# Performance work log

Hardware: AMD Instinct MI355X
Metric: run time of the kernel (lower is better)

## Reference

```python
import jax, jax.numpy as jnp
import numpy as np

IMG_H, IMG_W = 240, 320
NEAR, FAR = 0.1, 10.0
CHUNK = 64  # triangles rasterized per scan step
CAM_K = np.array([[286.2057, 0.0, 162.6306],
                  [0.0, 286.7852, 121.0245],
                  [0.0, 0.0, 1.0]], np.float32)


def build_projection(cam, w, h, x0=0, y0=0, nc=NEAR, fc=FAR):
    q = -(fc + nc) / float(fc - nc)
    qn = -2.0 * fc * nc / float(fc - nc)
    proj = np.array([
        [2 * cam[0, 0] / w, -2 * cam[0, 1] / w, (-2 * cam[0, 2] + w + 2 * x0) / w, 0],
        [0, -2 * cam[1, 1] / h, (-2 * cam[1, 2] + h + 2 * y0) / h, 0],
        [0, 0, q, qn],
        [0, 0, -1, 0]], dtype=np.float64)
    proj[1, :] *= -1.0
    return jnp.asarray(proj.T, jnp.float32)


def vertex_normals(verts, faces):
    # per-face normal scattered to its vertices then renormalized
    # (equals dirt lighting.vertex_normals_pre_split on split meshes)
    v0, v1, v2 = verts[faces[:, 0]], verts[faces[:, 1]], verts[faces[:, 2]]
    fn = jnp.cross(v1 - v0, v2 - v0)
    fn = fn / jnp.maximum(jnp.linalg.norm(fn, axis=1, keepdims=True), 1e-12)
    vn = (jnp.zeros_like(verts)
          .at[faces[:, 0]].add(fn)
          .at[faces[:, 1]].add(fn)
          .at[faces[:, 2]].add(fn))
    return vn / jnp.maximum(jnp.linalg.norm(vn, axis=1, keepdims=True), 1e-12)


def transform_vertices(vertices, pose, faces, proj):
    vert_obj = jnp.concatenate([vertices, jnp.ones_like(vertices[:, -1:])], axis=1)  # [V,4]
    normals = vertex_normals(vert_obj[:, :3], faces)
    gl = jnp.array([[1., 0., 0.], [0., -1., 0.], [0., 0., -1.]], jnp.float32)
    rot = gl @ pose[:3, :3]
    # replicate the flat-list surgery: cam_pose[:3,:3]=gl@R, negate t_y, t_z
    cam_pose = pose.at[:3, :3].set(rot).at[1, 3].multiply(-1.0).at[2, 3].multiply(-1.0)
    view = cam_pose.T
    vert_cam = vert_obj @ view                                   # [V,4]
    vert_3d = vert_obj[:, :3] @ pose[:3, :3].T + pose[:3, 3]     # [V,3]
    vert_clip = vert_cam @ proj                                  # [V,4]
    return vert_obj, vert_3d, vert_clip, normals


def rasterise(vert_clip, colors, faces, H, W):
    # z-buffered triangle rasterization with perspective-correct barycentric
    # interpolation, processed in chunks of CHUNK triangles via lax.scan.
    eps = 1e-9
    wc = vert_clip[:, 3]
    inv_w = 1.0 / jnp.where(jnp.abs(wc) > eps, wc, eps)
    ndc = vert_clip[:, :3] * inv_w[:, None]
    px = (ndc[:, 0] + 1.0) * 0.5 * W   # screen x
    py = (1.0 - ndc[:, 1]) * 0.5 * H   # screen y (row 0 at top)
    pz = ndc[:, 2]

    tpx, tpy, tpz = px[faces], py[faces], pz[faces]   # [F,3]
    tiw = inv_w[faces]                                # [F,3]
    tcol = colors[faces]                              # [F,3,C]
    tval = jnp.all(wc[faces] > 1e-6, axis=1)          # all verts in front

    F = faces.shape[0]
    pad = (-F) % CHUNK
    def padf(a):
        if pad == 0:
            return a
        return jnp.concatenate([a, jnp.zeros((pad,) + a.shape[1:], a.dtype)], 0)
    tpx, tpy, tpz, tiw, tcol = padf(tpx), padf(tpy), padf(tpz), padf(tiw), padf(tcol)
    tval = padf(tval)
    n_steps = (F + pad) // CHUNK
    resh = lambda a: a.reshape((n_steps, CHUNK) + a.shape[1:])
    xs = tuple(map(resh, (tpx, tpy, tpz, tiw, tcol, tval)))

    Xg = (jnp.arange(W, dtype=jnp.float32) + 0.5)[None, :, None]  # pixel centers
    Yg = (jnp.arange(H, dtype=jnp.float32) + 0.5)[:, None, None]
    BIG = jnp.float32(1e9)

    def step(carry, chunk):
        zbuf, cbuf = carry
        cpx, cpy, cpz, ciw, ccol, cval = chunk
        ax, ay = cpx[:, 0], cpy[:, 0]
        bx, by = cpx[:, 1], cpy[:, 1]
        cx, cy = cpx[:, 2], cpy[:, 2]
        area = (bx - ax) * (cy - ay) - (by - ay) * (cx - ax)            # [Fc]
        inv_area = 1.0 / jnp.where(jnp.abs(area) > 1e-12, area, 1e-12)
        # normalized edge functions (barycentrics), [H,W,Fc]
        e0 = ((Xg - bx) * (cy - by) - (Yg - by) * (cx - bx)) * inv_area
        e1 = ((Xg - cx) * (ay - cy) - (Yg - cy) * (ax - cx)) * inv_area
        e2 = 1.0 - e0 - e1
        depth = e0 * cpz[:, 0] + e1 * cpz[:, 1] + e2 * cpz[:, 2]        # screen-linear z
        inside = ((e0 >= 0) & (e1 >= 0) & (e2 >= 0) & cval
                  & (jnp.abs(area) > 1e-12) & (depth >= -1.0) & (depth <= 1.0))
        dmask = jnp.where(inside, depth, BIG)
        best = jnp.argmin(dmask, axis=2)                                # [H,W]
        bidx = best[..., None]
        bdepth = jnp.take_along_axis(dmask, bidx, 2)[..., 0]
        take = bdepth < zbuf
        b0 = jnp.take_along_axis(e0, bidx, 2)[..., 0]
        b1 = jnp.take_along_axis(e1, bidx, 2)[..., 0]
        b2 = 1.0 - b0 - b1
        piw = jnp.stack([b0, b1, b2], -1) * ciw[best]                   # [H,W,3]
        den = jnp.sum(piw, -1, keepdims=True)
        den = jnp.where(jnp.abs(den) > 1e-12, den, 1e-12)
        col = jnp.einsum('hwk,hwkc->hwc', piw / den, ccol[best])        # persp-correct
        zbuf = jnp.where(take, bdepth, zbuf)
        cbuf = jnp.where(take[..., None], col, cbuf)
        return (zbuf, cbuf), None

    zbuf0 = jnp.full((H, W), BIG, jnp.float32)
    cbuf0 = jnp.zeros((H, W, colors.shape[1]), jnp.float32)
    (_, cbuf), _ = jax.lax.scan(jax.checkpoint(step), (zbuf0, cbuf0), xs)
    return cbuf


def setup_inputs() -> dict:
    key = jax.random.key(0)
    k1, k2 = jax.random.split(key)
    V, F = 12288, 4096
    vertices = 0.15 * jax.random.normal(k1, (1, V, 3), jnp.float32)
    faces = jax.random.randint(k2, (1, F, 3), 0, V, jnp.int32)
    pose = jnp.eye(4, dtype=jnp.float32).at[2, 3].set(0.6)  # object 0.6m in front
    return {"vertices": vertices, "faces": faces, "poses": pose[None]}


def reference(vertices, faces, poses):
    proj = build_projection(CAM_K, IMG_W, IMG_H)
    faces0 = jnp.asarray(faces[0], jnp.int32)
    vert_obj, vert_3d, vert_clip, normals = transform_vertices(vertices[0], poses[0], faces0, proj)
    colors = jnp.concatenate(
        [jnp.ones_like(vert_obj[:, :1]), vert_3d, normals, vert_obj], axis=1)  # [V,11]
    g = rasterise(vert_clip, colors, faces0, IMG_H, IMG_W)  # [H,W,11]
    return g[None]
```

## Files before the change

kernel.cpp:

```cpp
#include <hip/hip_runtime.h>
#include <math.h>

#pragma clang fp contract(off)

#define IMG_H 240
#define IMG_W 320
#define NPX   (IMG_H * IMG_W)
#define NCH   11
#define NCHP  12
#define NSLICE 8
#define CULL_M 1e-3f
#define EZ_M   1e-5f

struct ProjM { float m[16]; };

extern "C" __global__ void k_init(float* __restrict__ vnacc, int n3v,
                                  unsigned long long* __restrict__ zkey) {
  int i = blockIdx.x * 256 + threadIdx.x;
  if (i < n3v) vnacc[i] = 0.0f;
  if (i < NPX) zkey[i] = ~0ull;
}

__device__ __forceinline__ void xform(float x, float y, float z,
                                      const float* __restrict__ pose,
                                      const ProjM& P,
                                      float& px, float& py, float& pz,
                                      float& iw, float& wc) {
  float c0 = ((x*pose[0]     + y*pose[1])     + z*pose[2])     + pose[3];
  float c1 = ((x*(-pose[4])  + y*(-pose[5]))  + z*(-pose[6]))  + (-pose[7]);
  float c2 = ((x*(-pose[8])  + y*(-pose[9]))  + z*(-pose[10])) + (-pose[11]);
  float c3 = ((x*pose[12]    + y*pose[13])    + z*pose[14])    + pose[15];
  float q0 = ((c0*P.m[0]  + c1*P.m[1])  + c2*P.m[2])  + c3*P.m[3];
  float q1 = ((c0*P.m[4]  + c1*P.m[5])  + c2*P.m[6])  + c3*P.m[7];
  float q2 = ((c0*P.m[8]  + c1*P.m[9])  + c2*P.m[10]) + c3*P.m[11];
  float q3 = ((c0*P.m[12] + c1*P.m[13]) + c2*P.m[14]) + c3*P.m[15];
  wc = q3;
  float denw = (fabsf(wc) > 1e-9f) ? wc : 1e-9f;
  iw = 1.0f / denw;
  float ndx = q0 * iw, ndy = q1 * iw;
  pz = q2 * iw;
  px = ((ndx + 1.0f) * 0.5f) * (float)IMG_W;
  py = ((1.0f - ndy) * 0.5f) * (float)IMG_H;
}

extern "C" __global__ void k_face(const float* __restrict__ verts,
                                  const int* __restrict__ faces,
                                  const float* __restrict__ pose,
                                  ProjM P,
                                  float* __restrict__ vnacc,
                                  float4* __restrict__ frec,
                                  float4* __restrict__ fbb,
                                  float4* __restrict__ fe,
                                  int4*  __restrict__ fidx, int F) {
  int f = blockIdx.x * 64 + threadIdx.x;
  if (f >= F) return;
  int i0 = faces[3*f+0], i1 = faces[3*f+1], i2 = faces[3*f+2];
  float x0 = verts[3*i0+0], y0 = verts[3*i0+1], z0 = verts[3*i0+2];
  float x1 = verts[3*i1+0], y1 = verts[3*i1+1], z1 = verts[3*i1+2];
  float x2 = verts[3*i2+0], y2 = verts[3*i2+1], z2 = verts[3*i2+2];

  {
    float ux = x1 - x0, uy = y1 - y0, uz = z1 - z0;
    float vx = x2 - x0, vy = y2 - y0, vz = z2 - z0;
    float fx = uy*vz - uz*vy;
    float fy = uz*vx - ux*vz;
    float fz = ux*vy - uy*vx;
    float n = sqrtf((fx*fx + fy*fy) + fz*fz);
    float d = fmaxf(n, 1e-12f);
    fx = fx / d; fy = fy / d; fz = fz / d;
    atomicAdd(&vnacc[3*i0+0], fx); atomicAdd(&vnacc[3*i0+1], fy); atomicAdd(&vnacc[3*i0+2], fz);
    atomicAdd(&vnacc[3*i1+0], fx); atomicAdd(&vnacc[3*i1+1], fy); atomicAdd(&vnacc[3*i1+2], fz);
    atomicAdd(&vnacc[3*i2+0], fx); atomicAdd(&vnacc[3*i2+1], fy); atomicAdd(&vnacc[3*i2+2], fz);
  }

  float ax, ay, pz0, iw0, w0;  xform(x0, y0, z0, pose, P, ax, ay, pz0, iw0, w0);
  float bx, by, pz1, iw1, w1;  xform(x1, y1, z1, pose, P, bx, by, pz1, iw1, w1);
  float cx, cy, pz2, iw2, w2;  xform(x2, y2, z2, pose, P, cx, cy, pz2, iw2, w2);

  float area = (bx - ax) * (cy - ay) - (by - ay) * (cx - ax);
  float inva = 1.0f / ((fabsf(area) > 1e-12f) ? area : 1e-12f);
  bool valid = (w0 > 1e-6f) && (w1 > 1e-6f) && (w2 > 1e-6f) && (fabsf(area) > 1e-12f);
  float rax = 2.0f*cx - ax, ray = 2.0f*cy - ay;
  float rbx = 2.0f*cx - bx, rby = 2.0f*cy - by;
  float minx = fminf(cx, fminf(rax, rbx)), maxx = fmaxf(cx, fmaxf(rax, rbx));
  float miny = fminf(cy, fminf(ray, rby)), maxy = fmaxf(cy, fmaxf(ray, rby));
  frec[4*f+0] = make_float4(bx, by, cy - by, cx - bx);
  frec[4*f+1] = make_float4(cx, cy, ay - cy, ax - cx);
  frec[4*f+2] = make_float4(inva, pz0, pz1, pz2);
  frec[4*f+3] = make_float4(iw0, iw1, iw2, 0.0f);
  fbb[f] = valid ? make_float4(minx, maxx, miny, maxy)
                 : make_float4(1e30f, -1e30f, 1e30f, -1e30f);
  fidx[f] = make_int4(i0, i1, i2, 0);
  {
    double dbx = bx, dby = by, dcx = cx, dcy = cy, dax = ax, day = ay;
    double dinv = (double)inva;
    double d0 = dcy - dby, d1 = dcx - dbx;
    double d2 = day - dcy, d3 = dax - dcx;
    double a0 = d0 * dinv, b0 = -d1 * dinv, c0 = (dby * d1 - dbx * d0) * dinv;
    double a1 = d2 * dinv, b1 = -d3 * dinv, c1 = (dcy * d3 - dcx * d2) * dinv;
    fe[2*f+0] = make_float4((float)a0, (float)b0, (float)c0, 0.0f);
    fe[2*f+1] = make_float4((float)a1, (float)b1, (float)c1, 0.0f);
  }
}

extern "C" __global__ void k_vertex(const float* __restrict__ verts,
                                    const float* __restrict__ vnacc,
                                    const float* __restrict__ pose,
                                    float4* __restrict__ colors, int V) {
  int i = blockIdx.x * 64 + threadIdx.x;
  if (i >= V) return;
  float x = verts[3*i+0], y = verts[3*i+1], z = verts[3*i+2];

  float nx = vnacc[3*i+0], ny = vnacc[3*i+1], nz = vnacc[3*i+2];
  float nn = sqrtf((nx*nx + ny*ny) + nz*nz);
  float nm = fmaxf(nn, 1e-12f);
  nx = nx / nm; ny = ny / nm; nz = nz / nm;

  float v3x = ((x*pose[0] + y*pose[1]) + z*pose[2])  + pose[3];
  float v3y = ((x*pose[4] + y*pose[5]) + z*pose[6])  + pose[7];
  float v3z = ((x*pose[8] + y*pose[9]) + z*pose[10]) + pose[11];

  colors[3*i+0] = make_float4(1.0f, v3x, v3y, v3z);
  colors[3*i+1] = make_float4(nx, ny, nz, x);
  colors[3*i+2] = make_float4(y, z, 1.0f, 0.0f);
}

extern "C" __global__ __launch_bounds__(256)
void k_rasterA(const float4* __restrict__ frec,
               const float4* __restrict__ fbb,
               const float4* __restrict__ fe,
               unsigned long long* __restrict__ zkey,
               int F, int nslice) {
  int t = threadIdx.x;
  int wave = t >> 6;
  int lane = t & 63;
  int sx = (wave & 1) * 8, sy = (wave >> 1) * 8;
  int pxi = blockIdx.x * 16 + sx + (lane & 7);
  int pyi = blockIdx.y * 16 + sy + (lane >> 3);
  float X = (float)pxi + 0.5f;
  float Y = (float)pyi + 0.5f;
  float tXlo = (float)(blockIdx.x * 16 + sx) + 0.5f, tXhi = tXlo + 7.0f;
  float tYlo = (float)(blockIdx.y * 16 + sy) + 0.5f, tYhi = tYlo + 7.0f;

  int f0 = blockIdx.z * nslice;
  int f1 = min(F, f0 + nslice);

  float bestd = 1e9f;
  int   besti = -1;

  for (int base = f0; base < f1; base += 64) {
    int f = base + lane;
    bool ov = false;
    if (f < f1) {
      float4 bb = fbb[f];
      ov = (bb.x - 1.0f <= tXhi) && (bb.y + 1.0f >= tXlo) &&
           (bb.z - 1.0f <= tYhi) && (bb.w + 1.0f >= tYlo);
      if (ov) {
        float4 E0 = fe[2*f+0];
        float4 E1 = fe[2*f+1];
        float pa0 = E0.x * tXlo, pb0 = E0.x * tXhi;
        float qa0 = E0.y * tYlo, qb0 = E0.y * tYhi;
        float e0mx = (fmaxf(pa0, pb0) + fmaxf(qa0, qb0)) + E0.z;
        float e0mn = (fminf(pa0, pb0) + fminf(qa0, qb0)) + E0.z;
        float pa1 = E1.x * tXlo, pb1 = E1.x * tXhi;
        float qa1 = E1.y * tYlo, qb1 = E1.y * tYhi;
        float e1mx = (fmaxf(pa1, pb1) + fmaxf(qa1, qb1)) + E1.z;
        float e1mn = (fminf(pa1, pb1) + fminf(qa1, qb1)) + E1.z;
        float e2mx = (1.0f - e0mn) - e1mn;
        ov = (e0mx >= -CULL_M) && (e1mx >= -CULL_M) && (e2mx >= -CULL_M);
      }
    }
    unsigned long long mask = __ballot(ov);

    while (mask) {
      int j = __builtin_ctzll(mask);
      mask &= mask - 1;
      int ju = __builtin_amdgcn_readfirstlane(base + j);
      const float4* fr = frec + (size_t)ju * 4;
      float4 C = fr[2];
      float zminf = fminf(C.y, fminf(C.z, C.w));
      if (__ballot(bestd > zminf - EZ_M) == 0ull) continue;
      float4 A = fr[0];
      float4 B = fr[1];
      float t0 = (X - A.x) * A.z;
      float t1 = (Y - A.y) * A.w;
      float e0 = (t0 - t1) * C.x;
      float t2 = (X - B.x) * B.z;
      float t3 = (Y - B.y) * B.w;
      float e1 = (t2 - t3) * C.x;
      float e2 = (1.0f - e0) - e1;
      float depth = ((e0 * C.y) + (e1 * C.z)) + (e2 * C.w);
      bool inside = (e0 >= 0.0f) && (e1 >= 0.0f) && (e2 >= 0.0f) &&
                    (depth >= -1.0f) && (depth <= 1.0f);
      if (inside && depth < bestd) {
        bestd = depth; besti = base + j;
      }
    }
  }

  if (besti >= 0) {
    unsigned int ub = __float_as_uint(bestd);
    ub = (ub & 0x80000000u) ? ~ub : (ub | 0x80000000u);
    unsigned long long key = ((unsigned long long)ub << 32) | (unsigned int)besti;
    atomicMin(&zkey[(size_t)pyi * IMG_W + pxi], key);
  }
}

extern "C" __global__ __launch_bounds__(256)
void k_resolve(const unsigned long long* __restrict__ zkey,
               const float4* __restrict__ frec,
               const float4* __restrict__ colors,
               const int4* __restrict__ fidx,
               float* __restrict__ out) {
  __shared__ float sOut[256 * NCH];
  int t = threadIdx.x;
  int p = blockIdx.x * 256 + t;
  int pyi = p / IMG_W, pxi = p - pyi * IMG_W;
  float X = (float)pxi + 0.5f;
  float Y = (float)pyi + 0.5f;
  unsigned long long key = zkey[p];

  float oc[NCH];
  if (key != ~0ull) {
    int besti = (int)(key & 0xFFFFFFFFu);
    const float4* fr = frec + (size_t)besti * 4;
    float4 A = fr[0], B = fr[1], C = fr[2], D = fr[3];
    float t0 = (X - A.x) * A.z;
    float t1 = (Y - A.y) * A.w;
    float e0 = (t0 - t1) * C.x;
    float t2 = (X - B.x) * B.z;
    float t3 = (Y - B.y) * B.w;
    float e1 = (t2 - t3) * C.x;
    float b2 = (1.0f - e0) - e1;
    float p0 = e0 * D.x, p1 = e1 * D.y, p2 = b2 * D.z;
    float den = (p0 + p1) + p2;
    if (!(fabsf(den) > 1e-12f)) den = 1e-12f;
    float u0 = p0 / den, u1 = p1 / den, u2 = p2 / den;
    int4 vi = fidx[besti];
    float c0v[NCHP], c1v[NCHP], c2v[NCHP];
    #pragma unroll
    for (int k = 0; k < 3; ++k) {
      *(float4*)(c0v + 4*k) = colors[3*vi.x + k];
      *(float4*)(c1v + 4*k) = colors[3*vi.y + k];
      *(float4*)(c2v + 4*k) = colors[3*vi.z + k];
    }
    #pragma unroll
    for (int ch = 0; ch < NCH; ++ch)
      oc[ch] = (u0 * c0v[ch] + u1 * c1v[ch]) + u2 * c2v[ch];
  } else {
    #pragma unroll
    for (int ch = 0; ch < NCH; ++ch) oc[ch] = 0.0f;
  }
  #pragma unroll
  for (int ch = 0; ch < NCH; ++ch) sOut[t * NCH + ch] = oc[ch];
  __syncthreads();
  float4* o4 = (float4*)(out + (size_t)blockIdx.x * 256 * NCH);
  const float4* s4 = (const float4*)sOut;
  #pragma unroll
  for (int k = 0; k < 3; ++k) {
    int idx = t + k * 256;
    if (idx < 704) o4[idx] = s4[idx];
  }
}

extern "C" void kernel_launch(void* const* d_in, const int* in_sizes, int n_in,
                              void* d_out, int out_size, void* d_ws, size_t ws_size,
                              hipStream_t stream) {
  const float* verts = (const float*)d_in[0];
  const int*   faces = (const int*)d_in[1];
  const float* pose  = (const float*)d_in[2];
  float* out = (float*)d_out;
  int V = in_sizes[0] / 3;
  int F = in_sizes[1] / 3;

  float* ws = (float*)d_ws;
  size_t o = 0;
  auto alloc = [&](size_t n) { size_t r = o; o += (n + 3) & ~(size_t)3; return r; };
  size_t o_zk   = alloc((size_t)2 * NPX);
  size_t o_vn   = alloc((size_t)3 * V);
  size_t o_col  = alloc((size_t)NCHP * V);
  size_t o_fr   = alloc((size_t)16 * F);
  size_t o_bb   = alloc((size_t)4 * F);
  size_t o_fe   = alloc((size_t)8 * F);
  size_t o_fi   = alloc((size_t)4 * F);
  unsigned long long* zkey = (unsigned long long*)(ws + o_zk);
  float*  vnacc = ws + o_vn;
  float4* col   = (float4*)(ws + o_col);
  float4* frec  = (float4*)(ws + o_fr);
  float4* fbb   = (float4*)(ws + o_bb);
  float4* fe    = (float4*)(ws + o_fe);
  int4*   fidx  = (int4*)(ws + o_fi);

  double fxd = 286.2057, sd = 0.0, cxd = 162.6306;
  double fyd = 286.7852, cyd = 121.0245;
  double wd = IMG_W, hd = IMG_H, ncd = 0.1, fcd = 10.0;
  double q  = -(fcd + ncd) / (fcd - ncd);
  double qn = -2.0 * fcd * ncd / (fcd - ncd);
  double Pd[16] = {
    2.0*fxd/wd, -2.0*sd/wd, (-2.0*cxd + wd)/wd, 0.0,
    0.0,        2.0*fyd/hd, (2.0*cyd - hd)/hd, -0.0,
    0.0,        0.0,        q,                  qn,
    0.0,        0.0,       -1.0,                0.0 };
  ProjM P;
  for (int i = 0; i < 16; ++i) P.m[i] = (float)Pd[i];

  int n3v = 3 * V;
  int initN = (NPX > n3v) ? NPX : n3v;
  k_init<<<(initN + 255) / 256, 256, 0, stream>>>(vnacc, n3v, zkey);
  k_face<<<(F + 63) / 64, 64, 0, stream>>>(verts, faces, pose, P, vnacc,
                                           frec, fbb, fe, fidx, F);
  k_vertex<<<(V + 63) / 64, 64, 0, stream>>>(verts, vnacc, pose, col, V);
  int nslice = (F + NSLICE - 1) / NSLICE;
  dim3 g(IMG_W / 16, IMG_H / 16, NSLICE);
  k_rasterA<<<g, 256, 0, stream>>>(frec, fbb, fe, zkey, F, nslice);
  k_resolve<<<NPX / 256, 256, 0, stream>>>(zkey, frec, col, fidx, out);
}
```

Measured before the change: 90.49 us.

## Sort faces front-to-back by depth bins and early-exit raster loop

Faces are bucketed into 256 bins by their minimum NDC depth using a histogram, a prefix scan and a scatter, so the rasterizer walks them roughly front to back. Each raster wave interleaves chunks across z-slices, reads the current per-pixel best depth from the global z-key buffer, and breaks once the remaining chunks' bin lower bound exceeds the wave's worst best depth. It also skips individual faces whose min depth cannot win. This adds three small kernels, extra global memory traffic and per-chunk atomics in exchange for culling occluded triangles.

```diff
diff --git a/kernel.cpp b/kernel.cpp
--- a/kernel.cpp
+++ b/kernel.cpp
@@ -11,14 +11,24 @@
 #define NSLICE 8
 #define CULL_M 1e-3f
 #define EZ_M   1e-5f
+#define NBIN   256
 
 struct ProjM { float m[16]; };
 
+__device__ __forceinline__ int zbin(float zm) {
+  float t = fminf(fmaxf((zm + 1.0f) * 128.0f, 0.0f), 255.0f);
+  int b = (int)t;
+  if ((float)b * 0.0078125f - 1.0f > zm) b = (b > 0) ? b - 1 : 0;
+  return b;
+}
+
 extern "C" __global__ void k_init(float* __restrict__ vnacc, int n3v,
-                                  unsigned long long* __restrict__ zkey) {
+                                  unsigned long long* __restrict__ zkey,
+                                  int* __restrict__ hist) {
   int i = blockIdx.x * 256 + threadIdx.x;
   if (i < n3v) vnacc[i] = 0.0f;
   if (i < NPX) zkey[i] = ~0ull;
+  if (i < NBIN) hist[i] = 0;
 }
 
 __device__ __forceinline__ void xform(float x, float y, float z,
@@ -51,7 +61,9 @@
                                   float4* __restrict__ frec,
                                   float4* __restrict__ fbb,
                                   float4* __restrict__ fe,
-                                  int4*  __restrict__ fidx, int F) {
+                                  int4*  __restrict__ fidx,
+                                  float* __restrict__ fzmin,
+                                  int*   __restrict__ hist, int F) {
   int f = blockIdx.x * 64 + threadIdx.x;
   if (f >= F) return;
   int i0 = faces[3*f+0], i1 = faces[3*f+1], i2 = faces[3*f+2];
@@ -91,6 +103,11 @@
   fbb[f] = valid ? make_float4(minx, maxx, miny, maxy)
                  : make_float4(1e30f, -1e30f, 1e30f, -1e30f);
   fidx[f] = make_int4(i0, i1, i2, 0);
+
+  float zm = valid ? fminf(pz0, fminf(pz1, pz2)) : __builtin_huge_valf();
+  fzmin[f] = zm;
+  atomicAdd(&hist[zbin(zm)], 1);
+
   {
     double dbx = bx, dby = by, dcx = cx, dcy = cy, dax = ax, day = ay;
     double dinv = (double)inva;
@@ -103,6 +120,44 @@
   }
 }
 
+extern "C" __global__ void k_scan(const int* __restrict__ hist,
+                                  int* __restrict__ binoff) {
+  __shared__ int s[NBIN];
+  int t = threadIdx.x;
+  int v = hist[t];
+  s[t] = v;
+  __syncthreads();
+  for (int o = 1; o < NBIN; o <<= 1) {
+    int x = (t >= o) ? s[t - o] : 0;
+    __syncthreads();
+    s[t] += x;
+    __syncthreads();
+  }
+  binoff[t] = s[t] - v;
+}
+
+extern "C" __global__ void k_scatter(const float* __restrict__ fzmin,
+                                     int* __restrict__ binoff,
+                                     const float4* __restrict__ fbb,
+                                     const float4* __restrict__ fe,
+                                     int*   __restrict__ forig,
+                                     float* __restrict__ szmin,
+                                     float* __restrict__ smon,
+                                     float4* __restrict__ fbbs,
+                                     float4* __restrict__ fes, int F) {
+  int f = blockIdx.x * 256 + threadIdx.x;
+  if (f >= F) return;
+  float zm = fzmin[f];
+  int b = zbin(zm);
+  int pos = atomicAdd(&binoff[b], 1);
+  forig[pos] = f;
+  szmin[pos] = zm;
+  smon[pos]  = (float)b * 0.0078125f - 1.0f;
+  fbbs[pos]  = fbb[f];
+  fes[2*pos+0] = fe[2*f+0];
+  fes[2*pos+1] = fe[2*f+1];
+}
+
 extern "C" __global__ void k_vertex(const float* __restrict__ verts,
                                     const float* __restrict__ vnacc,
                                     const float* __restrict__ pose,
@@ -127,10 +182,13 @@
 
 extern "C" __global__ __launch_bounds__(256)
 void k_rasterA(const float4* __restrict__ frec,
-               const float4* __restrict__ fbb,
-               const float4* __restrict__ fe,
+               const float4* __restrict__ fbbs,
+               const float4* __restrict__ fes,
+               const int*    __restrict__ forig,
+               const float*  __restrict__ szmin,
+               const float*  __restrict__ smon,
                unsigned long long* __restrict__ zkey,
-               int F, int nslice) {
+               int F) {
   int t = threadIdx.x;
   int wave = t >> 6;
   int lane = t & 63;
@@ -141,47 +199,63 @@
   float Y = (float)pyi + 0.5f;
   float tXlo = (float)(blockIdx.x * 16 + sx) + 0.5f, tXhi = tXlo + 7.0f;
   float tYlo = (float)(blockIdx.y * 16 + sy) + 0.5f, tYhi = tYlo + 7.0f;
-
-  int f0 = blockIdx.z * nslice;
-  int f1 = min(F, f0 + nslice);
-
-  float bestd = 1e9f;
+  size_t pix = (size_t)pyi * IMG_W + pxi;
+
+  float bestd = 1.0f + 1.0e-3f;
   int   besti = -1;
 
-  for (int base = f0; base < f1; base += 64) {
-    int f = base + lane;
+  int nchunk = (F + 63) >> 6;
+  for (int c = blockIdx.z; c < nchunk; c += NSLICE) {
+    int base = c << 6;
+
+    float pb = bestd;
+    {
+      unsigned long long k = __hip_atomic_load(&zkey[pix], __ATOMIC_RELAXED,
+                                               __HIP_MEMORY_SCOPE_AGENT);
+      if (k != ~0ull) {
+        unsigned int ub = (unsigned int)(k >> 32);
+        unsigned int fb = (ub & 0x80000000u) ? (ub & 0x7FFFFFFFu) : ~ub;
+        pb = fminf(pb, __uint_as_float(fb));
+      }
+    }
+    float pbm = pb;
+    #pragma unroll
+    for (int o = 32; o > 0; o >>= 1) pbm = fmaxf(pbm, __shfl_xor(pbm, o));
+
+    if (pbm <= smon[base] - EZ_M) break;
+
+    int i = base + lane;
     bool ov = false;
-    if (f < f1) {
-      float4 bb = fbb[f];
+    if (i < F && szmin[i] < pbm + EZ_M) {
+      float4 bb = fbbs[i];
       ov = (bb.x - 1.0f <= tXhi) && (bb.y + 1.0f >= tXlo) &&
            (bb.z - 1.0f <= tYhi) && (bb.w + 1.0f >= tYlo);
       if (ov) {
-        float4 E0 = fe[2*f+0];
-        float4 E1 = fe[2*f+1];
+        float4 E0 = fes[2*i+0];
+        float4 E1 = fes[2*i+1];
         float pa0 = E0.x * tXlo, pb0 = E0.x * tXhi;
         float qa0 = E0.y * tYlo, qb0 = E0.y * tYhi;
         float e0mx = (fmaxf(pa0, pb0) + fmaxf(qa0, qb0)) + E0.z;
-        float e0mn = (fminf(pa0, pb0) + fminf(qa0, qb0)) + E0.z;
         float pa1 = E1.x * tXlo, pb1 = E1.x * tXhi;
         float qa1 = E1.y * tYlo, qb1 = E1.y * tYhi;
         float e1mx = (fmaxf(pa1, pb1) + fmaxf(qa1, qb1)) + E1.z;
+        float e0mn = (fminf(pa0, pb0) + fminf(qa0, qb0)) + E0.z;
         float e1mn = (fminf(pa1, pb1) + fminf(qa1, qb1)) + E1.z;
         float e2mx = (1.0f - e0mn) - e1mn;
         ov = (e0mx >= -CULL_M) && (e1mx >= -CULL_M) && (e2mx >= -CULL_M);
       }
     }
     unsigned long long mask = __ballot(ov);
+    bool improved = false;
 
     while (mask) {
       int j = __builtin_ctzll(mask);
       mask &= mask - 1;
-      int ju = __builtin_amdgcn_readfirstlane(base + j);
+      int ju = __builtin_amdgcn_readfirstlane(forig[base + j]);
       const float4* fr = frec + (size_t)ju * 4;
-      float4 C = fr[2];
-      float zminf = fminf(C.y, fminf(C.z, C.w));
-      if (__ballot(bestd > zminf - EZ_M) == 0ull) continue;
       float4 A = fr[0];
       float4 B = fr[1];
+      float4 C = fr[2];
       float t0 = (X - A.x) * A.z;
       float t1 = (Y - A.y) * A.w;
       float e0 = (t0 - t1) * C.x;
@@ -193,16 +267,16 @@
       bool inside = (e0 >= 0.0f) && (e1 >= 0.0f) && (e2 >= 0.0f) &&
                     (depth >= -1.0f) && (depth <= 1.0f);
       if (inside && depth < bestd) {
-        bestd = depth; besti = base + j;
+        bestd = depth; besti = ju; improved = true;
       }
     }
-  }
-
-  if (besti >= 0) {
-    unsigned int ub = __float_as_uint(bestd);
-    ub = (ub & 0x80000000u) ? ~ub : (ub | 0x80000000u);
-    unsigned long long key = ((unsigned long long)ub << 32) | (unsigned int)besti;
-    atomicMin(&zkey[(size_t)pyi * IMG_W + pxi], key);
+
+    if (improved && bestd <= pb) {
+      unsigned int ub = __float_as_uint(bestd);
+      ub = (ub & 0x80000000u) ? ~ub : (ub | 0x80000000u);
+      unsigned long long key = ((unsigned long long)ub << 32) | (unsigned int)besti;
+      atomicMin(&zkey[pix], key);
+    }
   }
 }
 
@@ -283,6 +357,14 @@
   size_t o_bb   = alloc((size_t)4 * F);
   size_t o_fe   = alloc((size_t)8 * F);
   size_t o_fi   = alloc((size_t)4 * F);
+  size_t o_fz   = alloc((size_t)F);
+  size_t o_hist = alloc((size_t)NBIN);
+  size_t o_boff = alloc((size_t)NBIN);
+  size_t o_fo   = alloc((size_t)F);
+  size_t o_sz   = alloc((size_t)F);
+  size_t o_sm   = alloc((size_t)F);
+  size_t o_bbs  = alloc((size_t)4 * F);
+  size_t o_fes  = alloc((size_t)8 * F);
   unsigned long long* zkey = (unsigned long long*)(ws + o_zk);
   float*  vnacc = ws + o_vn;
   float4* col   = (float4*)(ws + o_col);
@@ -290,6 +372,14 @@
   float4* fbb   = (float4*)(ws + o_bb);
   float4* fe    = (float4*)(ws + o_fe);
   int4*   fidx  = (int4*)(ws + o_fi);
+  float*  fzmin = ws + o_fz;
+  int*    hist  = (int*)(ws + o_hist);
+  int*    boff  = (int*)(ws + o_boff);
+  int*    forig = (int*)(ws + o_fo);
+  float*  szmin = ws + o_sz;
+  float*  smon  = ws + o_sm;
+  float4* fbbs  = (float4*)(ws + o_bbs);
+  float4* fes   = (float4*)(ws + o_fes);
 
   double fxd = 286.2057, sd = 0.0, cxd = 162.6306;
   double fyd = 286.7852, cyd = 121.0245;
@@ -306,12 +396,14 @@
 
   int n3v = 3 * V;
   int initN = (NPX > n3v) ? NPX : n3v;
-  k_init<<<(initN + 255) / 256, 256, 0, stream>>>(vnacc, n3v, zkey);
+  k_init<<<(initN + 255) / 256, 256, 0, stream>>>(vnacc, n3v, zkey, hist);
   k_face<<<(F + 63) / 64, 64, 0, stream>>>(verts, faces, pose, P, vnacc,
-                                           frec, fbb, fe, fidx, F);
+                                           frec, fbb, fe, fidx, fzmin, hist, F);
+  k_scan<<<1, NBIN, 0, stream>>>(hist, boff);
+  k_scatter<<<(F + 255) / 256, 256, 0, stream>>>(fzmin, boff, fbb, fe,
+                                                 forig, szmin, smon, fbbs, fes, F);
   k_vertex<<<(V + 63) / 64, 64, 0, stream>>>(verts, vnacc, pose, col, V);
-  int nslice = (F + NSLICE - 1) / NSLICE;
   dim3 g(IMG_W / 16, IMG_H / 16, NSLICE);
-  k_rasterA<<<g, 256, 0, stream>>>(frec, fbb, fe, zkey, F, nslice);
+  k_rasterA<<<g, 256, 0, stream>>>(frec, fbbs, fes, forig, szmin, smon, zkey, F);
   k_resolve<<<NPX / 256, 256, 0, stream>>>(zkey, frec, col, fidx, out);
 }
```

Result: slower. 103.1 us (+13.9%).
